# Kernel tuning notes

Measured on AMD Instinct MI355X. Metric: run time of the kernel, lower is better.

## Reference

```python
import jax, jax.numpy as jnp
import numpy as np

N_NODES = 50000
N_EDGES = 1600000


def gcn_conv(x, edge_index, W, b):
    """PyG GCNConv: linear transform, add self-loops, symmetric deg^-1/2 norm, scatter-add."""
    n = x.shape[0]
    h = x @ W  # [N, out]
    loop = jnp.arange(n)
    src = jnp.concatenate([edge_index[0], loop])
    dst = jnp.concatenate([edge_index[1], loop])
    ones = jnp.ones(src.shape[0], dtype=h.dtype)
    deg = jax.ops.segment_sum(ones, dst, num_segments=n)  # in-degree incl. self-loop
    dinv = jnp.where(deg > 0, jax.lax.rsqrt(deg), 0.0)
    norm = dinv[src] * dinv[dst]  # [E+N]
    msg = h[src] * norm[:, None]  # gathered, normalized messages
    out = jax.ops.segment_sum(msg, dst, num_segments=n)
    return out + b


def setup_inputs() -> dict:
    key = jax.random.key(0)
    k1, k2, k3, k4 = jax.random.split(key, 4)
    x = jax.random.normal(k1, (N_NODES, 512), dtype=jnp.float32)
    edge_index = jax.random.randint(k2, (2, N_EDGES), 0, N_NODES, dtype=jnp.int64)
    W1 = jax.random.normal(k3, (512, 128), dtype=jnp.float32) * (1.0 / np.sqrt(512))
    b1 = jnp.zeros((128,), dtype=jnp.float32)
    W2 = jax.random.normal(k4, (128, 40), dtype=jnp.float32) * (1.0 / np.sqrt(128))
    b2 = jnp.zeros((40,), dtype=jnp.float32)
    return {"x": x, "edge_index": edge_index, "W1": W1, "b1": b1, "W2": W2, "b2": b2}


def reference(x, edge_index, W1, b1, W2, b2):
    h = gcn_conv(x, edge_index, W1, b1)
    h = jax.nn.relu(h)
    h = gcn_conv(h, edge_index, W2, b2)
    return jax.nn.log_softmax(h, axis=1)
```

## Files before the change

### kernel.cpp

```cpp
#include <hip/hip_runtime.h>
#include <hip/hip_bf16.h>
#include <math.h>


#define FEAT1 512
#define FEAT2 128
#define FEAT3 40

typedef __attribute__((ext_vector_type(8))) short bf16x8;
typedef __attribute__((ext_vector_type(4))) float f32x4;

__device__ __forceinline__ unsigned short f2bf(float f) {
    union { float f; unsigned u; } c; c.f = f;
    unsigned r = c.u + 0x7fff + ((c.u >> 16) & 1);
    return (unsigned short)(r >> 16);
}
__device__ __forceinline__ float bf2f(unsigned v16) {
    union { unsigned u; float f; } c; c.u = v16 << 16;
    return c.f;
}

__device__ __forceinline__ bf16x8 pack_bf8(f32x4 a, f32x4 b) {
    bf16x8 r;
    r[0] = (short)f2bf(a[0]); r[1] = (short)f2bf(a[1]);
    r[2] = (short)f2bf(a[2]); r[3] = (short)f2bf(a[3]);
    r[4] = (short)f2bf(b[0]); r[5] = (short)f2bf(b[1]);
    r[6] = (short)f2bf(b[2]); r[7] = (short)f2bf(b[3]);
    return r;
}

__global__ void detect_i64_kernel(const int* __restrict__ ei, int* flagp) {
    __shared__ int any;
    if (threadIdx.x == 0) any = 0;
    __syncthreads();
    int v = ei[2 * threadIdx.x + 1];
    if (v != 0) any = 1;
    __syncthreads();
    if (threadIdx.x == 0) *flagp = (any == 0) ? 1 : 0;
}

__device__ __forceinline__ int load_src(const int* ei, long e, long E, int f64) {
    return f64 ? ei[2 * e] : ei[e];
}
__device__ __forceinline__ int load_dst(const int* ei, long e, long E, int f64) {
    return f64 ? ei[2 * E + 2 * e] : ei[E + e];
}

__launch_bounds__(1024)
__global__ void partA_kernel(const int* __restrict__ ei, const int* __restrict__ flagp,
                             int* __restrict__ gbkt, unsigned* __restrict__ part,
                             int bktCap, long E, int NB) {
    __shared__ int hist[256], lbase[256], lcur[256];
    int f64 = *flagp;
    int t = threadIdx.x;
    long chunk = (E + gridDim.x - 1) / gridDim.x;
    long start = (long)blockIdx.x * chunk;
    long end = start + chunk; if (end > E) end = E;
    if (t < 256) { hist[t] = 0; lcur[t] = 0; }
    __syncthreads();

    for (long e0 = start; e0 < end; e0 += 1024) {
        long e = e0 + t;
        if (e < end) {
            int dst = load_dst(ei, e, E, f64);
            atomicAdd(&hist[dst >> 8], 1);
        }
    }
    __syncthreads();
    if (t < NB && hist[t]) lbase[t] = atomicAdd(&gbkt[t], hist[t]);
    __syncthreads();

    for (long e0 = start; e0 < end; e0 += 1024) {
        long e = e0 + t;
        if (e < end) {
            int src = load_src(ei, e, E, f64);
            int dst = load_dst(ei, e, E, f64);
            int bkt = dst >> 8;
            int pos = lbase[bkt] + atomicAdd(&lcur[bkt], 1);
            if (pos < bktCap)
                part[(long)bkt * bktCap + pos] = (unsigned)src | ((unsigned)(dst & 255) << 17);
        }
    }
}

__global__ void bscan_kernel(const int* __restrict__ gbkt, int* __restrict__ bktBase,
                             int* __restrict__ offsets, int NB, int N, int E) {
    __shared__ int s[256];
    int t = threadIdx.x;
    int v = (t < NB) ? gbkt[t] : 0;
    s[t] = v;
    __syncthreads();
    #pragma unroll
    for (int d = 1; d < 256; d <<= 1) {
        int tv = (t >= d) ? s[t - d] : 0;
        __syncthreads();
        s[t] += tv;
        __syncthreads();
    }
    bktBase[t] = s[t] - v;
    if (t == 0) offsets[N] = E;
}

__launch_bounds__(256)
__global__ void partB_kernel(const unsigned* __restrict__ part, int bktCap,
                             const int* __restrict__ gbkt, const int* __restrict__ bktBase,
                             int* __restrict__ offsets, float* __restrict__ dinv,
                             int* __restrict__ col, int N) {
    __shared__ int h[256], sc[256], cur[256];
    int b = blockIdx.x, t = threadIdx.x;
    int n = gbkt[b]; if (n > bktCap) n = bktCap;
    int base = bktBase[b];
    int lo = b << 8;
    const unsigned* p = part + (long)b * bktCap;
    h[t] = 0;
    __syncthreads();
    for (int i = t; i < n; i += 256) atomicAdd(&h[(p[i] >> 17) & 255], 1);
    __syncthreads();
    int cnt = h[t];
    sc[t] = cnt;
    __syncthreads();
    #pragma unroll
    for (int d = 1; d < 256; d <<= 1) {
        int tv = (t >= d) ? sc[t - d] : 0;
        __syncthreads();
        sc[t] += tv;
        __syncthreads();
    }
    int ex = sc[t] - cnt;
    int node = lo + t;
    if (node < N) {
        offsets[node] = base + ex;
        dinv[node] = 1.0f / sqrtf((float)(cnt + 1));
    }
    cur[t] = ex;
    __syncthreads();
    for (int i = t; i < n; i += 256) {
        unsigned u = p[i];
        int r = atomicAdd(&cur[(u >> 17) & 255], 1);
        col[base + r] = u & 0x1FFFF;
    }
}

__global__ void w1bt_kernel(const float* __restrict__ W1, unsigned short* __restrict__ Bt) {
    int n = blockIdx.x;
    for (int k = threadIdx.x; k < FEAT1; k += blockDim.x)
        Bt[(long)n * FEAT1 + k] = f2bf(W1[(long)k * FEAT2 + n]);
}

__global__ void w2bt_kernel(const float* __restrict__ W2, unsigned short* __restrict__ Bt2) {
    int n = blockIdx.x;
    for (int k = threadIdx.x; k < FEAT2; k += blockDim.x)
        Bt2[(long)n * FEAT2 + k] = (n < FEAT3) ? f2bf(W2[(long)k * FEAT3 + n]) : 0;
}

__launch_bounds__(256)
__global__ void gemm1_reg_kernel(const float* __restrict__ A,
                                 const unsigned short* __restrict__ Bt,
                                 const float* __restrict__ dinv,
                                 unsigned short* __restrict__ C, int M) {
    int wave = blockIdx.x * 4 + (threadIdx.x >> 6);
    int lane = threadIdx.x & 63;
    int quad = lane >> 4, r15 = lane & 15;
    int row0 = wave * 16;
    if (row0 >= M) return;
    int arow = row0 + r15;
    if (arow >= M) arow = M - 1;
    const float* ap = A + (long)arow * FEAT1 + quad * 8;
    const unsigned short* bp = Bt + (long)r15 * FEAT1 + quad * 8;

    f32x4 raw[16];
    #pragma unroll
    for (int ks = 0; ks < 8; ks++) {
        raw[2 * ks]     = *(const f32x4*)(ap + ks * 32);
        raw[2 * ks + 1] = *(const f32x4*)(ap + ks * 32 + 4);
    }

    f32x4 acc[8];
    #pragma unroll
    for (int nt = 0; nt < 8; nt++) acc[nt] = (f32x4){0.f, 0.f, 0.f, 0.f};

    bf16x8 af[8];
    #pragma unroll
    for (int ks = 0; ks < 8; ks++) af[ks] = pack_bf8(raw[2 * ks], raw[2 * ks + 1]);

    #pragma unroll
    for (int ks = 0; ks < 8; ks++) {
        raw[2 * ks]     = *(const f32x4*)(ap + 256 + ks * 32);
        raw[2 * ks + 1] = *(const f32x4*)(ap + 256 + ks * 32 + 4);
    }

    #pragma unroll
    for (int ks = 0; ks < 8; ks++) {
        #pragma unroll
        for (int nt = 0; nt < 8; nt++) {
            bf16x8 bfrag = *(const bf16x8*)(bp + (long)nt * 16 * FEAT1 + ks * 32);
            acc[nt] = __builtin_amdgcn_mfma_f32_16x16x32_bf16(af[ks], bfrag, acc[nt], 0, 0, 0);
        }
    }

    #pragma unroll
    for (int ks = 0; ks < 8; ks++) af[ks] = pack_bf8(raw[2 * ks], raw[2 * ks + 1]);

    #pragma unroll
    for (int ks = 0; ks < 8; ks++) {
        #pragma unroll
        for (int nt = 0; nt < 8; nt++) {
            bf16x8 bfrag = *(const bf16x8*)(bp + (long)nt * 16 * FEAT1 + 256 + ks * 32);
            acc[nt] = __builtin_amdgcn_mfma_f32_16x16x32_bf16(af[ks], bfrag, acc[nt], 0, 0, 0);
        }
    }

    #pragma unroll
    for (int reg = 0; reg < 4; reg++) {
        int orow = row0 + quad * 4 + reg;
        if (orow >= M) continue;
        float di = dinv[orow];
        #pragma unroll
        for (int nt = 0; nt < 8; nt++)
            C[(long)orow * FEAT2 + nt * 16 + r15] = f2bf(acc[nt][reg] * di);
    }
}

__launch_bounds__(256)
__global__ void agg1_kernel(const unsigned short* __restrict__ h1s,
                            const int* __restrict__ col, const int* __restrict__ off,
                            const float* __restrict__ dinv, const float* __restrict__ b1,
                            unsigned short* __restrict__ a1, int N) {
    int node = blockIdx.x * 4 + (threadIdx.x >> 6);
    if (node >= N) return;
    int l = threadIdx.x & 63;
    int o0 = off[node], o1 = off[node + 1];
    float ax = 0.f, ay = 0.f;
    for (int base = o0; base < o1; base += 64) {
        int cnt = min(64, o1 - base);
        int myc = (l < cnt) ? col[base + l] : 0;
        int e = 0;
        for (; e + 4 <= cnt; e += 4) {
            int s0 = __shfl(myc, e + 0);
            int s1 = __shfl(myc, e + 1);
            int s2 = __shfl(myc, e + 2);
            int s3 = __shfl(myc, e + 3);
            unsigned p0 = *(const unsigned*)(h1s + (long)s0 * FEAT2 + 2 * l);
            unsigned p1 = *(const unsigned*)(h1s + (long)s1 * FEAT2 + 2 * l);
            unsigned p2 = *(const unsigned*)(h1s + (long)s2 * FEAT2 + 2 * l);
            unsigned p3 = *(const unsigned*)(h1s + (long)s3 * FEAT2 + 2 * l);
            ax += bf2f(p0 & 0xffffu) + bf2f(p1 & 0xffffu) +
                  bf2f(p2 & 0xffffu) + bf2f(p3 & 0xffffu);
            ay += bf2f(p0 >> 16) + bf2f(p1 >> 16) + bf2f(p2 >> 16) + bf2f(p3 >> 16);
        }
        for (; e < cnt; ++e) {
            int s = __shfl(myc, e);
            unsigned p = *(const unsigned*)(h1s + (long)s * FEAT2 + 2 * l);
            ax += bf2f(p & 0xffffu);
            ay += bf2f(p >> 16);
        }
    }
    unsigned pv = *(const unsigned*)(h1s + (long)node * FEAT2 + 2 * l);
    ax += bf2f(pv & 0xffffu);
    ay += bf2f(pv >> 16);
    float di = dinv[node];
    float2 b = *(const float2*)(b1 + 2 * l);
    float vx = ax * di + b.x;
    float vy = ay * di + b.y;
    vx = vx > 0.f ? vx : 0.f;
    vy = vy > 0.f ? vy : 0.f;
    *(unsigned*)(a1 + (long)node * FEAT2 + 2 * l) =
        (unsigned)f2bf(vx) | ((unsigned)f2bf(vy) << 16);
}

__launch_bounds__(256)
__global__ void gemm2_mfma_kernel(const unsigned short* __restrict__ A,
                                  const unsigned short* __restrict__ Bt2,
                                  const float* __restrict__ dinv,
                                  unsigned short* __restrict__ C, int M) {
    int wave = blockIdx.x * (blockDim.x >> 6) + (threadIdx.x >> 6);
    int lane = threadIdx.x & 63;
    int quad = lane >> 4, r15 = lane & 15;
    int row0 = wave * 16;
    if (row0 >= M) return;
    int arow = row0 + r15;
    if (arow >= M) arow = M - 1;

    bf16x8 af[4];
    const unsigned short* ap = A + (long)arow * FEAT2 + quad * 8;
    #pragma unroll
    for (int ks = 0; ks < 4; ks++) af[ks] = *(const bf16x8*)(ap + ks * 32);

    f32x4 acc[3];
    #pragma unroll
    for (int nt = 0; nt < 3; nt++) acc[nt] = (f32x4){0.f, 0.f, 0.f, 0.f};
    #pragma unroll
    for (int ks = 0; ks < 4; ks++) {
        #pragma unroll
        for (int nt = 0; nt < 3; nt++) {
            bf16x8 bf = *(const bf16x8*)(Bt2 + (long)(nt * 16 + r15) * FEAT2 + ks * 32 + quad * 8);
            acc[nt] = __builtin_amdgcn_mfma_f32_16x16x32_bf16(af[ks], bf, acc[nt], 0, 0, 0);
        }
    }

    #pragma unroll
    for (int reg = 0; reg < 4; reg++) {
        int orow = row0 + quad * 4 + reg;
        if (orow >= M) continue;
        float di = dinv[orow];
        #pragma unroll
        for (int nt = 0; nt < 3; nt++) {
            int ocol = nt * 16 + r15;
            if (ocol < FEAT3)
                C[(long)orow * FEAT3 + ocol] = f2bf(acc[nt][reg] * di);
        }
    }
}

__launch_bounds__(256)
__global__ void agg2_lsm_kernel(const unsigned short* __restrict__ h2s,
                                const int* __restrict__ col, const int* __restrict__ off,
                                const float* __restrict__ dinv, const float* __restrict__ b2,
                                float* __restrict__ out, int N) {
    int node = blockIdx.x * 4 + (threadIdx.x >> 6);
    if (node >= N) return;
    int l = threadIdx.x & 63;
    bool act = l < FEAT3 / 2;
    int o0 = off[node], o1 = off[node + 1];
    float ax = 0.f, ay = 0.f;
    for (int base = o0; base < o1; base += 64) {
        int cnt = min(64, o1 - base);
        int myc = (l < cnt) ? col[base + l] : 0;
        int e = 0;
        for (; e + 4 <= cnt; e += 4) {
            int s0 = __shfl(myc, e + 0);
            int s1 = __shfl(myc, e + 1);
            int s2 = __shfl(myc, e + 2);
            int s3 = __shfl(myc, e + 3);
            if (act) {
                unsigned p0 = *(const unsigned*)(h2s + (long)s0 * FEAT3 + 2 * l);
                unsigned p1 = *(const unsigned*)(h2s + (long)s1 * FEAT3 + 2 * l);
                unsigned p2 = *(const unsigned*)(h2s + (long)s2 * FEAT3 + 2 * l);
                unsigned p3 = *(const unsigned*)(h2s + (long)s3 * FEAT3 + 2 * l);
                ax += bf2f(p0 & 0xffffu) + bf2f(p1 & 0xffffu) +
                      bf2f(p2 & 0xffffu) + bf2f(p3 & 0xffffu);
                ay += bf2f(p0 >> 16) + bf2f(p1 >> 16) + bf2f(p2 >> 16) + bf2f(p3 >> 16);
            }
        }
        for (; e < cnt; ++e) {
            int s = __shfl(myc, e);
            if (act) {
                unsigned p = *(const unsigned*)(h2s + (long)s * FEAT3 + 2 * l);
                ax += bf2f(p & 0xffffu);
                ay += bf2f(p >> 16);
            }
        }
    }
    float vx = -INFINITY, vy = -INFINITY;
    if (act) {
        unsigned pv = *(const unsigned*)(h2s + (long)node * FEAT3 + 2 * l);
        float di = dinv[node];
        float2 b = *(const float2*)(b2 + 2 * l);
        vx = (ax + bf2f(pv & 0xffffu)) * di + b.x;
        vy = (ay + bf2f(pv >> 16)) * di + b.y;
    }
    float m = fmaxf(vx, vy);
    #pragma unroll
    for (int o = 32; o >= 1; o >>= 1) m = fmaxf(m, __shfl_xor(m, o));
    float e = act ? (expf(vx - m) + expf(vy - m)) : 0.f;
    #pragma unroll
    for (int o = 32; o >= 1; o >>= 1) e += __shfl_xor(e, o);
    float ls = logf(e);
    if (act) {
        *(float2*)(out + (long)node * FEAT3 + 2 * l) = make_float2(vx - m - ls, vy - m - ls);
    }
}

extern "C" void kernel_launch(void* const* d_in, const int* in_sizes, int n_in,
                              void* d_out, int out_size, void* d_ws, size_t ws_size,
                              hipStream_t stream) {
    const float* x  = (const float*)d_in[0];
    const int*   ei = (const int*)d_in[1];
    const float* W1 = (const float*)d_in[2];
    const float* b1 = (const float*)d_in[3];
    const float* W2 = (const float*)d_in[4];
    const float* b2 = (const float*)d_in[5];
    float* out = (float*)d_out;

    const int  N = in_sizes[0] / FEAT1;
    const long E = in_sizes[1] / 2;

    char* ws = (char*)d_ws;
    size_t off = 0;
    auto alloc = [&](size_t bytes) -> void* {
        off = (off + 255) & ~(size_t)255;
        void* p = ws + off;
        off += bytes;
        return p;
    };
    const int NB = (N + 255) >> 8;
    const int bktCap = (int)(E / NB) + 1024;
    int*   offsets = (int*)alloc((size_t)(N + 1) * 4);
    float* dinv    = (float*)alloc((size_t)N * 4);
    int*   col     = (int*)alloc((size_t)E * 4);
    unsigned short* h1s = (unsigned short*)alloc((size_t)N * FEAT2 * 2);
    unsigned short* a1  = (unsigned short*)alloc((size_t)N * FEAT2 * 2);
    unsigned short* h2s = (unsigned short*)alloc((size_t)N * FEAT3 * 2);
    unsigned short* Bt  = (unsigned short*)alloc((size_t)FEAT2 * FEAT1 * 2);
    unsigned short* Bt2 = (unsigned short*)alloc((size_t)48 * FEAT2 * 2);
    unsigned* part = (unsigned*)alloc((size_t)NB * bktCap * 4);
    int*   gbkt    = (int*)alloc(256 * 4);
    int*   bktBase = (int*)alloc(256 * 4);
    int*   flagp   = (int*)alloc(4);

    detect_i64_kernel<<<1, 256, 0, stream>>>(ei, flagp);
    hipMemsetAsync(gbkt, 0, 256 * 4, stream);
    partA_kernel<<<256, 1024, 0, stream>>>(ei, flagp, gbkt, part, bktCap, E, NB);
    bscan_kernel<<<1, 256, 0, stream>>>(gbkt, bktBase, offsets, NB, N, (int)E);
    partB_kernel<<<NB, 256, 0, stream>>>(part, bktCap, gbkt, bktBase, offsets, dinv, col, N);

    w1bt_kernel<<<FEAT2, 256, 0, stream>>>(W1, Bt);
    w2bt_kernel<<<48, 128, 0, stream>>>(W2, Bt2);
    {
        int waves = (N + 15) / 16;
        gemm1_reg_kernel<<<(waves + 3) / 4, 256, 0, stream>>>(x, Bt, dinv, h1s, N);
    }
    agg1_kernel<<<(N + 3) / 4, 256, 0, stream>>>(h1s, col, offsets, dinv, b1, a1, N);
    gemm2_mfma_kernel<<<(N / 16 + 3) / 4, 256, 0, stream>>>(a1, Bt2, dinv, h2s, N);
    agg2_lsm_kernel<<<(N + 3) / 4, 256, 0, stream>>>(h2s, col, offsets, dinv, b2, out, N);
}
```

Measured before the change: 368.4 us.

## Stage swizzled W1 in LDS for gemm1 and pipeline A loads

```diff
diff --git a/kernel.cpp b/kernel.cpp
--- a/kernel.cpp
+++ b/kernel.cpp
@@ -21,12 +21,12 @@
 }
 
 __device__ __forceinline__ bf16x8 pack_bf8(f32x4 a, f32x4 b) {
-    bf16x8 r;
-    r[0] = (short)f2bf(a[0]); r[1] = (short)f2bf(a[1]);
-    r[2] = (short)f2bf(a[2]); r[3] = (short)f2bf(a[3]);
-    r[4] = (short)f2bf(b[0]); r[5] = (short)f2bf(b[1]);
-    r[6] = (short)f2bf(b[2]); r[7] = (short)f2bf(b[3]);
-    return r;
+    union { __hip_bfloat162 h[4]; bf16x8 v; } u;
+    u.h[0] = __float22bfloat162_rn(make_float2(a[0], a[1]));
+    u.h[1] = __float22bfloat162_rn(make_float2(a[2], a[3]));
+    u.h[2] = __float22bfloat162_rn(make_float2(b[0], b[1]));
+    u.h[3] = __float22bfloat162_rn(make_float2(b[2], b[3]));
+    return u.v;
 }
 
 __global__ void detect_i64_kernel(const int* __restrict__ ei, int* flagp) {
@@ -142,9 +142,13 @@
 }
 
 __global__ void w1bt_kernel(const float* __restrict__ W1, unsigned short* __restrict__ Bt) {
-    int n = blockIdx.x;
-    for (int k = threadIdx.x; k < FEAT1; k += blockDim.x)
-        Bt[(long)n * FEAT1 + k] = f2bf(W1[(long)k * FEAT2 + n]);
+    int r = blockIdx.x;
+    int x7 = r & 7;
+    for (int k = threadIdx.x; k < FEAT1; k += blockDim.x) {
+        int c = k >> 3, j = k & 7;
+        int eo = (((c ^ x7) << 3) | j);
+        Bt[(long)r * FEAT1 + eo] = f2bf(W1[(long)k * FEAT2 + r]);
+    }
 }
 
 __global__ void w2bt_kernel(const float* __restrict__ W2, unsigned short* __restrict__ Bt2) {
@@ -153,71 +157,72 @@
         Bt2[(long)n * FEAT2 + k] = (n < FEAT3) ? f2bf(W2[(long)k * FEAT3 + n]) : 0;
 }
 
-__launch_bounds__(256)
-__global__ void gemm1_reg_kernel(const float* __restrict__ A,
-                                 const unsigned short* __restrict__ Bt,
-                                 const float* __restrict__ dinv,
-                                 unsigned short* __restrict__ C, int M) {
-    int wave = blockIdx.x * 4 + (threadIdx.x >> 6);
-    int lane = threadIdx.x & 63;
+#define G1_NW 8
+__launch_bounds__(512, 2)
+__global__ void gemm1_mfma_kernel(const float* __restrict__ A,
+                                  const unsigned short* __restrict__ Bsw,
+                                  const float* __restrict__ dinv,
+                                  unsigned short* __restrict__ C, int M) {
+    __shared__ unsigned short Bl[FEAT2 * FEAT1];
+    int t = threadIdx.x;
+
+    {
+        uint4 tmp[16];
+        #pragma unroll
+        for (int r = 0; r < 16; r++)
+            tmp[r] = *(const uint4*)((const char*)Bsw + (size_t)t * 16 + (size_t)r * 8192);
+        #pragma unroll
+        for (int r = 0; r < 16; r++)
+            *(uint4*)((char*)Bl + (size_t)t * 16 + (size_t)r * 8192) = tmp[r];
+    }
+    __syncthreads();
+
+    int wave = blockIdx.x * G1_NW + (t >> 6);
+    int lane = t & 63;
     int quad = lane >> 4, r15 = lane & 15;
     int row0 = wave * 16;
-    if (row0 >= M) return;
-    int arow = row0 + r15;
-    if (arow >= M) arow = M - 1;
-    const float* ap = A + (long)arow * FEAT1 + quad * 8;
-    const unsigned short* bp = Bt + (long)r15 * FEAT1 + quad * 8;
-
-    f32x4 raw[16];
-    #pragma unroll
-    for (int ks = 0; ks < 8; ks++) {
-        raw[2 * ks]     = *(const f32x4*)(ap + ks * 32);
-        raw[2 * ks + 1] = *(const f32x4*)(ap + ks * 32 + 4);
-    }
-
-    f32x4 acc[8];
-    #pragma unroll
-    for (int nt = 0; nt < 8; nt++) acc[nt] = (f32x4){0.f, 0.f, 0.f, 0.f};
-
-    bf16x8 af[8];
-    #pragma unroll
-    for (int ks = 0; ks < 8; ks++) af[ks] = pack_bf8(raw[2 * ks], raw[2 * ks + 1]);
-
-    #pragma unroll
-    for (int ks = 0; ks < 8; ks++) {
-        raw[2 * ks]     = *(const f32x4*)(ap + 256 + ks * 32);
-        raw[2 * ks + 1] = *(const f32x4*)(ap + 256 + ks * 32 + 4);
-    }
-
-    #pragma unroll
-    for (int ks = 0; ks < 8; ks++) {
-        #pragma unroll
-        for (int nt = 0; nt < 8; nt++) {
-            bf16x8 bfrag = *(const bf16x8*)(bp + (long)nt * 16 * FEAT1 + ks * 32);
-            acc[nt] = __builtin_amdgcn_mfma_f32_16x16x32_bf16(af[ks], bfrag, acc[nt], 0, 0, 0);
-        }
-    }
-
-    #pragma unroll
-    for (int ks = 0; ks < 8; ks++) af[ks] = pack_bf8(raw[2 * ks], raw[2 * ks + 1]);
-
-    #pragma unroll
-    for (int ks = 0; ks < 8; ks++) {
-        #pragma unroll
-        for (int nt = 0; nt < 8; nt++) {
-            bf16x8 bfrag = *(const bf16x8*)(bp + (long)nt * 16 * FEAT1 + 256 + ks * 32);
-            acc[nt] = __builtin_amdgcn_mfma_f32_16x16x32_bf16(af[ks], bfrag, acc[nt], 0, 0, 0);
-        }
-    }
-
-    #pragma unroll
-    for (int reg = 0; reg < 4; reg++) {
-        int orow = row0 + quad * 4 + reg;
-        if (orow >= M) continue;
-        float di = dinv[orow];
-        #pragma unroll
-        for (int nt = 0; nt < 8; nt++)
-            C[(long)orow * FEAT2 + nt * 16 + r15] = f2bf(acc[nt][reg] * di);
+    if (row0 < M) {
+        int arow = row0 + r15;
+        if (arow >= M) arow = M - 1;
+        const float* ap = A + (long)arow * FEAT1 + quad * 8;
+        int x7 = r15 & 7;
+
+        f32x4 ra[4][2];
+        #pragma unroll
+        for (int p = 0; p < 3; p++) {
+            ra[p][0] = *(const f32x4*)(ap + p * 32);
+            ra[p][1] = *(const f32x4*)(ap + p * 32 + 4);
+        }
+
+        f32x4 acc[8];
+        #pragma unroll
+        for (int nt = 0; nt < 8; nt++) acc[nt] = (f32x4){0.f, 0.f, 0.f, 0.f};
+
+        #pragma unroll
+        for (int ks = 0; ks < 16; ks++) {
+            if (ks < 13) {
+                ra[(ks + 3) & 3][0] = *(const f32x4*)(ap + (ks + 3) * 32);
+                ra[(ks + 3) & 3][1] = *(const f32x4*)(ap + (ks + 3) * 32 + 4);
+            }
+            bf16x8 af = pack_bf8(ra[ks & 3][0], ra[ks & 3][1]);
+            #pragma unroll
+            for (int nt = 0; nt < 8; nt++) {
+                int eo = (nt * 16 + r15) * FEAT1 + (((ks * 4 + quad) ^ x7) << 3);
+                bf16x8 bfrag = *(const bf16x8*)(Bl + eo);
+                acc[nt] = __builtin_amdgcn_mfma_f32_16x16x32_bf16(af, bfrag, acc[nt], 0, 0, 0);
+            }
+        }
+
+        #pragma unroll
+        for (int reg = 0; reg < 4; reg++) {
+            int orow = row0 + quad * 4 + reg;
+            if (orow < M) {
+                float di = dinv[orow];
+                #pragma unroll
+                for (int nt = 0; nt < 8; nt++)
+                    C[(long)orow * FEAT2 + nt * 16 + r15] = f2bf(acc[nt][reg] * di);
+            }
+        }
     }
 }
 
@@ -417,8 +422,9 @@
     w1bt_kernel<<<FEAT2, 256, 0, stream>>>(W1, Bt);
     w2bt_kernel<<<48, 128, 0, stream>>>(W2, Bt2);
     {
-        int waves = (N + 15) / 16;
-        gemm1_reg_kernel<<<(waves + 3) / 4, 256, 0, stream>>>(x, Bt, dinv, h1s, N);
+        int waves  = (N + 15) / 16;
+        int blocks = (waves + G1_NW - 1) / G1_NW;
+        gemm1_mfma_kernel<<<blocks, 512, 0, stream>>>(x, Bt, dinv, h1s, N);
     }
     agg1_kernel<<<(N + 3) / 4, 256, 0, stream>>>(h1s, col, offsets, dinv, b1, a1, N);
     gemm2_mfma_kernel<<<(N / 16 + 3) / 4, 256, 0, stream>>>(a1, Bt2, dinv, h2s, N);
```

Result: faster. 331.4 us (-10.0%).
